# Kernel tuning notes

Measured on AMD Instinct MI355X. Metric: run time of the kernel, lower is better.

The kernel has to match this reference:

```python
import jax, jax.numpy as jnp
import numpy as np

EPS = 1e-7          # keras.backend.epsilon()
L2_EPS = 1e-12      # tf.math.l2_normalize epsilon


def _l2_normalize(v):
    # tf.math.l2_normalize: v * rsqrt(max(sum(v^2), 1e-12))
    sq = jnp.sum(v * v, axis=-1, keepdims=True)
    return v * jax.lax.rsqrt(jnp.maximum(sq, L2_EPS))


def setup_inputs() -> dict:
    key = jax.random.key(0)
    k1, k2 = jax.random.split(key)
    x = jax.random.normal(k1, (4, 2048, 1024), dtype=jnp.float32)
    ref = jax.random.normal(k2, (8192, 1024), dtype=jnp.float32)
    return {"x": x, "ref": ref}


def reference(x, ref):
    # inputs += K.epsilon()
    xn = _l2_normalize(x + EPS)          # [B, N, D]
    refn = _l2_normalize(ref)            # [M, D]
    # fused form of sum(xn[..., N, 1, D] * refn[1, M, D], axis=-1) -> [B, N, M]
    return jnp.einsum('bnd,md->bnm', xn, refn)
```

## Files before the change

### kernel.cpp

```cpp
#include <hip/hip_runtime.h>
#include <hip/hip_bf16.h>
#include <stdint.h>

typedef __bf16 bf16x8 __attribute__((ext_vector_type(8)));
typedef float f32x4 __attribute__((ext_vector_type(4)));

#define GLB_AS __attribute__((address_space(1)))
#define LDS_AS __attribute__((address_space(3)))

__device__ __forceinline__ void gload_lds16(const void* g, void* l) {
    __builtin_amdgcn_global_load_lds((GLB_AS void*)(g), (LDS_AS void*)(l), 16, 0, 0);
}

#define GM 8192
#define GN 8192
#define GK 1024
#define NT (GK / 64)
#define NI (NT / 2)

__global__ __launch_bounds__(256) void normalize_rows(
    const float* __restrict__ x, const float* __restrict__ ref,
    __bf16* __restrict__ outA, __bf16* __restrict__ outB)
{
    const int row = blockIdx.x;
    const bool isX = row < 8192;
    const size_t r = isX ? (size_t)row : (size_t)(row - 8192);
    const float* src = isX ? (x + r * 1024) : (ref + r * 1024);
    __bf16* dst = isX ? (outA + r * 1024) : (outB + r * 1024);
    const float eps = isX ? 1e-7f : 0.0f;

    const int t = threadIdx.x;
    float4 v = reinterpret_cast<const float4*>(src)[t];
    v.x += eps; v.y += eps; v.z += eps; v.w += eps;
    float ss = v.x * v.x + v.y * v.y + v.z * v.z + v.w * v.w;

    #pragma unroll
    for (int o = 32; o; o >>= 1) ss += __shfl_xor(ss, o, 64);

    __shared__ float red[4];
    const int wv = t >> 6, lane = t & 63;
    if (lane == 0) red[wv] = ss;
    __syncthreads();
    const float tot = red[0] + red[1] + red[2] + red[3];
    const float inv = rsqrtf(fmaxf(tot, 1e-12f));

    __bf16 b[4];
    b[0] = (__bf16)(v.x * inv);
    b[1] = (__bf16)(v.y * inv);
    b[2] = (__bf16)(v.z * inv);
    b[3] = (__bf16)(v.w * inv);
    uint2 pk;
    __builtin_memcpy(&pk, b, 8);
    reinterpret_cast<uint2*>(dst)[t] = pk;
}

__global__ __launch_bounds__(512, 2) void gemm_v9(
    const __bf16* __restrict__ A, const __bf16* __restrict__ B,
    float* __restrict__ C)
{
    __shared__ __bf16 As[2][2][128][64];
    __shared__ __bf16 Bs[2][2][128][64];

    const int bid = blockIdx.x;
    const int swz = (bid & 7) * 128 + (bid >> 3);
    const int within = swz & 15;
    const int super  = swz >> 4;
    const int tm = (super & 7) * 4 + (within & 3);
    const int tn = (super >> 3) * 4 + (within >> 2);
    const size_t rowM0 = (size_t)tm * 256;
    const size_t rowN0 = (size_t)tn * 256;

    const int tid  = threadIdx.x;
    const int wave = tid >> 6;
    const int lane = tid & 63;
    const int wr = wave >> 2;
    const int wc = wave & 3;

    const int srow  = lane >> 3;
    const int sslot = (lane & 7) ^ srow;
    const int fr = lane & 15;
    const int fs = lane >> 4;

    int woffA[4][2], woffB[2][2];
    #pragma unroll
    for (int m = 0; m < 4; ++m) {
        const int l = wr * 64 + m * 16 + fr;
        #pragma unroll
        for (int ks = 0; ks < 2; ++ks)
            woffA[m][ks] = l * 128 + (((ks * 4 + fs) ^ (l & 7)) * 16);
    }
    #pragma unroll
    for (int n = 0; n < 2; ++n) {
        const int l = wc * 32 + n * 16 + fr;
        #pragma unroll
        for (int ks = 0; ks < 2; ++ks)
            woffB[n][ks] = l * 128 + (((ks * 4 + fs) ^ (l & 7)) * 16);
    }

    bf16x8 af[4][2];
    bf16x8 bq[2][2][2];
    f32x4  acc[8][4] = {};

#define STAGE_A(T, h, b) { \
    _Pragma("unroll") \
    for (int j = 0; j < 2; ++j) { \
        const size_t grow = rowM0 + (size_t)(j) * 128 + (h) * 64 + wave * 8 + srow; \
        const char* src = (const char*)A + (grow * GK + (size_t)(T) * 64) * 2 + sslot * 16; \
        char* dst = (char*)&As[b][h][0][0] + (j * 64 + wave * 8) * 128; \
        gload_lds16(src, dst); } }

#define STAGE_B(T, h, b) { \
    _Pragma("unroll") \
    for (int j = 0; j < 2; ++j) { \
        const int l = j * 64 + wave * 8 + srow; \
        const size_t grow = rowN0 + (size_t)(l >> 5) * 64 + (h) * 32 + (l & 31); \
        const char* src = (const char*)B + (grow * GK + (size_t)(T) * 64) * 2 + sslot * 16; \
        char* dst = (char*)&Bs[b][h][0][0] + (j * 64 + wave * 8) * 128; \
        gload_lds16(src, dst); } }

#define LDA(qm, b) { \
    _Pragma("unroll") \
    for (int m = 0; m < 4; ++m) \
    _Pragma("unroll") \
    for (int ks = 0; ks < 2; ++ks) \
        af[m][ks] = *(const bf16x8*)((const char*)&As[b][qm][0][0] + woffA[m][ks]); }

#define LDB(qn, b) { \
    _Pragma("unroll") \
    for (int n = 0; n < 2; ++n) \
    _Pragma("unroll") \
    for (int ks = 0; ks < 2; ++ks) \
        bq[qn][n][ks] = *(const bf16x8*)((const char*)&Bs[b][qn][0][0] + woffB[n][ks]); }

#define QMFMA(qm, qn) { \
    __builtin_amdgcn_s_setprio(1); \
    _Pragma("unroll") \
    for (int ks = 0; ks < 2; ++ks) \
    _Pragma("unroll") \
    for (int m = 0; m < 4; ++m) \
    _Pragma("unroll") \
    for (int n = 0; n < 2; ++n) \
        acc[(qm) * 4 + m][(qn) * 2 + n] = __builtin_amdgcn_mfma_f32_16x16x32_bf16( \
            bq[qn][n][ks], af[m][ks], acc[(qm) * 4 + m][(qn) * 2 + n], 0, 0, 0); \
    __builtin_amdgcn_s_setprio(0); }

#define STORE_QUAD(qm, qn) { \
    _Pragma("unroll") \
    for (int m = 0; m < 4; ++m) \
    _Pragma("unroll") \
    for (int n = 0; n < 2; ++n) { \
        const size_t row = rowM0 + (size_t)wr * 128 + (qm) * 64 + m * 16 + (lane & 15); \
        const size_t col = rowN0 + (size_t)wc * 64 + (qn) * 32 + n * 16 + (lane >> 4) * 4; \
        *reinterpret_cast<f32x4*>(&C[row * (size_t)GN + col]) = acc[(qm) * 4 + m][(qn) * 2 + n]; } }

#define BAR() __builtin_amdgcn_s_barrier()
#define LGKM8()  asm volatile("s_waitcnt lgkmcnt(8)")
#define LGKM0()  asm volatile("s_waitcnt lgkmcnt(0)")
#define VM(n)    asm volatile("s_waitcnt vmcnt(" #n ")" ::: "memory")

    STAGE_A(0, 0, 0); STAGE_A(0, 1, 0); STAGE_B(0, 0, 0); STAGE_B(0, 1, 0);
    STAGE_A(1, 0, 1); STAGE_B(1, 0, 1); STAGE_B(1, 1, 1);
    VM(6);
    BAR();

    #pragma unroll 1
    for (int i = 0; i < NI; ++i) {
        const int t1 = 2 * i + 1, t2 = 2 * i + 2, t3 = 2 * i + 3;
        const bool more = (i < NI - 1);

        LDA(0, 0); LDB(0, 0);
        STAGE_A(t1, 1, 1);
        LGKM8();
        BAR(); LGKM0();
        QMFMA(0, 0);
        BAR();
        LDB(1, 0);
        if (more) STAGE_A(t2, 0, 0);
        BAR(); LGKM0();
        QMFMA(0, 1);
        BAR();
        LDA(1, 0);
        if (more) STAGE_B(t2, 0, 0);
        BAR(); LGKM0();
        QMFMA(1, 0);
        BAR();
        if (more) { STAGE_B(t2, 1, 0); VM(6); }
        else      { VM(0); }
        BAR();
        QMFMA(1, 1);
        BAR();
        LDA(0, 1); LDB(0, 1);
        if (more) STAGE_A(t2, 1, 0);
        LGKM8();
        BAR(); LGKM0();
        QMFMA(0, 0);
        BAR();
        LDB(1, 1);
        if (more) STAGE_A(t3, 0, 1);
        BAR(); LGKM0();
        QMFMA(0, 1);
        BAR();
        LDA(1, 1);
        if (more) STAGE_B(t3, 0, 1);
        BAR(); LGKM0();
        QMFMA(1, 0);
        BAR();
        if (more) {
            STAGE_B(t3, 1, 1); VM(6);
            BAR();
            QMFMA(1, 1);
            BAR();
        } else {
            QMFMA(1, 1);
        }
    }

    STORE_QUAD(0, 0); STORE_QUAD(0, 1); STORE_QUAD(1, 0); STORE_QUAD(1, 1);

#undef STAGE_A
#undef STAGE_B
#undef LDA
#undef LDB
#undef QMFMA
#undef STORE_QUAD
#undef BAR
#undef LGKM8
#undef LGKM0
#undef VM
}

__global__ __launch_bounds__(256) void naive_pairwise(
    const float* __restrict__ x, const float* __restrict__ ref,
    float* __restrict__ out)
{
    const int row = blockIdx.x >> 5;
    const int j = (blockIdx.x & 31) * 256 + threadIdx.x;
    const float* xr = x + (size_t)row * 1024;
    const float* rr = ref + (size_t)j * 1024;

    __shared__ float xs[1024];
    float part = 0.f;
    for (int k = threadIdx.x; k < 1024; k += 256) {
        float v = xr[k] + 1e-7f;
        xs[k] = v;
        part += v * v;
    }
    #pragma unroll
    for (int o = 32; o; o >>= 1) part += __shfl_xor(part, o, 64);
    __shared__ float red[4];
    if ((threadIdx.x & 63) == 0) red[threadIdx.x >> 6] = part;
    __syncthreads();
    const float ssx = red[0] + red[1] + red[2] + red[3];

    float ssr = 0.f, dot = 0.f;
    for (int k = 0; k < 1024; ++k) {
        float r = rr[k];
        ssr += r * r;
        dot += r * xs[k];
    }
    out[(size_t)row * 8192 + j] =
        dot * rsqrtf(fmaxf(ssx, 1e-12f)) * rsqrtf(fmaxf(ssr, 1e-12f));
}

extern "C" void kernel_launch(void* const* d_in, const int* in_sizes, int n_in,
                              void* d_out, int out_size, void* d_ws, size_t ws_size,
                              hipStream_t stream) {
    const float* x   = (const float*)d_in[0];
    const float* ref = (const float*)d_in[1];
    float* out = (float*)d_out;

    const size_t need = (size_t)GM * GK * sizeof(__bf16) * 2;
    if (ws_size >= need) {
        __bf16* wsA = (__bf16*)d_ws;
        __bf16* wsB = wsA + (size_t)GM * GK;
        normalize_rows<<<16384, 256, 0, stream>>>(x, ref, wsA, wsB);
        gemm_v9<<<(GM / 256) * (GN / 256), 512, 0, stream>>>(wsA, wsB, out);
    } else {
        naive_pairwise<<<8192 * 32, 256, 0, stream>>>(x, ref, out);
    }
}
```

Measured before the change: 185.9 us.

## Interleave LDS fragment reads with MFMA via sched_group_barrier software pipelining

Restructures the GEMM main loop so the LDS fragment loads for the next quadrant are issued inside the current quadrant's MFMA block. sched_group_barrier interleaves groups of 4 MFMAs with DS reads, and the explicit lgkmcnt waits are removed. The first quadrant's loads are hoisted before the loop and rotated to the end of each iteration. This is meant to hide LDS read latency behind matrix math and drop some barrier stalls. It relies on compiler-inserted waitcnts and register double-buffering of fragments, which may raise register pressure or reorder loads unexpectedly.

Result: slower. 391.5 us (+110.6%).

```diff
diff --git a/kernel.cpp b/kernel.cpp
--- a/kernel.cpp
+++ b/kernel.cpp
@@ -54,7 +54,7 @@
     reinterpret_cast<uint2*>(dst)[t] = pk;
 }
 
-__global__ __launch_bounds__(512, 2) void gemm_v9(
+__global__ __launch_bounds__(512, 2) void gemm_v10(
     const __bf16* __restrict__ A, const __bf16* __restrict__ B,
     float* __restrict__ C)
 {
@@ -132,17 +132,21 @@
     for (int ks = 0; ks < 2; ++ks) \
         bq[qn][n][ks] = *(const bf16x8*)((const char*)&Bs[b][qn][0][0] + woffB[n][ks]); }
 
-#define QMFMA(qm, qn) { \
-    __builtin_amdgcn_s_setprio(1); \
+#define MF16(qm, qn) { \
+    _Pragma("unroll") \
+    for (int m = 0; m < 4; ++m) \
     _Pragma("unroll") \
     for (int ks = 0; ks < 2; ++ks) \
-    _Pragma("unroll") \
-    for (int m = 0; m < 4; ++m) \
     _Pragma("unroll") \
     for (int n = 0; n < 2; ++n) \
         acc[(qm) * 4 + m][(qn) * 2 + n] = __builtin_amdgcn_mfma_f32_16x16x32_bf16( \
-            bq[qn][n][ks], af[m][ks], acc[(qm) * 4 + m][(qn) * 2 + n], 0, 0, 0); \
-    __builtin_amdgcn_s_setprio(0); }
+            bq[qn][n][ks], af[m][ks], acc[(qm) * 4 + m][(qn) * 2 + n], 0, 0, 0); }
+
+#define SGB_M4   __builtin_amdgcn_sched_group_barrier(0x008, 4, 0)
+#define SGB_D(n) __builtin_amdgcn_sched_group_barrier(0x100, n, 0)
+#define WEAVE3() { SGB_M4; SGB_D(3); SGB_M4; SGB_D(3); SGB_M4; SGB_D(3); SGB_M4; SGB_D(3); }
+#define WEAVE2() { SGB_M4; SGB_D(2); SGB_M4; SGB_D(2); SGB_M4; SGB_D(2); SGB_M4; SGB_D(2); }
+#define WEAVE1() { SGB_M4; SGB_D(1); SGB_M4; SGB_D(1); SGB_M4; SGB_D(1); SGB_M4; SGB_D(1); }
 
 #define STORE_QUAD(qm, qn) { \
     _Pragma("unroll") \
@@ -153,65 +157,59 @@
         const size_t col = rowN0 + (size_t)wc * 64 + (qn) * 32 + n * 16 + (lane >> 4) * 4; \
         *reinterpret_cast<f32x4*>(&C[row * (size_t)GN + col]) = acc[(qm) * 4 + m][(qn) * 2 + n]; } }
 
-#define BAR() __builtin_amdgcn_s_barrier()
-#define LGKM8()  asm volatile("s_waitcnt lgkmcnt(8)")
-#define LGKM0()  asm volatile("s_waitcnt lgkmcnt(0)")
-#define VM(n)    asm volatile("s_waitcnt vmcnt(" #n ")" ::: "memory")
+#define BAR()  __builtin_amdgcn_s_barrier()
+#define PRIO1() __builtin_amdgcn_s_setprio(1)
+#define PRIO0() __builtin_amdgcn_s_setprio(0)
+#define VM(n)  asm volatile("s_waitcnt vmcnt(" #n ")" ::: "memory")
 
     STAGE_A(0, 0, 0); STAGE_A(0, 1, 0); STAGE_B(0, 0, 0); STAGE_B(0, 1, 0);
     STAGE_A(1, 0, 1); STAGE_B(1, 0, 1); STAGE_B(1, 1, 1);
     VM(6);
     BAR();
+    LDA(0, 0); LDB(0, 0);
 
     #pragma unroll 1
     for (int i = 0; i < NI; ++i) {
         const int t1 = 2 * i + 1, t2 = 2 * i + 2, t3 = 2 * i + 3;
         const bool more = (i < NI - 1);
 
-        LDA(0, 0); LDB(0, 0);
         STAGE_A(t1, 1, 1);
-        LGKM8();
-        BAR(); LGKM0();
-        QMFMA(0, 0);
-        BAR();
-        LDB(1, 0);
+        BAR();
+        PRIO1(); MF16(0, 0); LDB(1, 0); WEAVE1(); PRIO0();
+        BAR();
         if (more) STAGE_A(t2, 0, 0);
-        BAR(); LGKM0();
-        QMFMA(0, 1);
-        BAR();
-        LDA(1, 0);
+        BAR();
+        PRIO1(); MF16(0, 1); LDA(1, 0); WEAVE2(); PRIO0();
+        BAR();
         if (more) STAGE_B(t2, 0, 0);
-        BAR(); LGKM0();
-        QMFMA(1, 0);
+        BAR();
+        PRIO1(); MF16(1, 0); PRIO0();
         BAR();
         if (more) { STAGE_B(t2, 1, 0); VM(6); }
         else      { VM(0); }
         BAR();
-        QMFMA(1, 1);
-        BAR();
-        LDA(0, 1); LDB(0, 1);
+        PRIO1(); MF16(1, 1); LDA(0, 1); LDB(0, 1); WEAVE3(); PRIO0();
+        BAR();
         if (more) STAGE_A(t2, 1, 0);
-        LGKM8();
-        BAR(); LGKM0();
-        QMFMA(0, 0);
-        BAR();
-        LDB(1, 1);
+        BAR();
+        PRIO1(); MF16(0, 0); LDB(1, 1); WEAVE1(); PRIO0();
+        BAR();
         if (more) STAGE_A(t3, 0, 1);
-        BAR(); LGKM0();
-        QMFMA(0, 1);
-        BAR();
-        LDA(1, 1);
+        BAR();
+        PRIO1(); MF16(0, 1); LDA(1, 1); WEAVE2(); PRIO0();
+        BAR();
         if (more) STAGE_B(t3, 0, 1);
-        BAR(); LGKM0();
-        QMFMA(1, 0);
+        BAR();
+        PRIO1(); MF16(1, 0); PRIO0();
         BAR();
         if (more) {
             STAGE_B(t3, 1, 1); VM(6);
             BAR();
-            QMFMA(1, 1);
+            PRIO1(); MF16(1, 1); LDA(0, 0); LDB(0, 0); WEAVE3(); PRIO0();
             BAR();
         } else {
-            QMFMA(1, 1);
+            BAR();
+            PRIO1(); MF16(1, 1); PRIO0();
         }
     }
 
@@ -221,11 +219,16 @@
 #undef STAGE_B
 #undef LDA
 #undef LDB
-#undef QMFMA
+#undef MF16
+#undef SGB_M4
+#undef SGB_D
+#undef WEAVE3
+#undef WEAVE2
+#undef WEAVE1
 #undef STORE_QUAD
 #undef BAR
-#undef LGKM8
-#undef LGKM0
+#undef PRIO1
+#undef PRIO0
 #undef VM
 }
 
@@ -274,7 +277,7 @@
         __bf16* wsA = (__bf16*)d_ws;
         __bf16* wsB = wsA + (size_t)GM * GK;
         normalize_rows<<<16384, 256, 0, stream>>>(x, ref, wsA, wsB);
-        gemm_v9<<<(GM / 256) * (GN / 256), 512, 0, stream>>>(wsA, wsB, out);
+        gemm_v10<<<(GM / 256) * (GN / 256), 512, 0, stream>>>(wsA, wsB, out);
     } else {
         naive_pairwise<<<8192 * 32, 256, 0, stream>>>(x, ref, out);
     }
```
